# Kernel tuning notes

Hardware: AMD Instinct MI355X
Metric: run time of the kernel (lower is better)

Reference implementation:

```python
import jax, jax.numpy as jnp
import numpy as np

D_MODEL = 256; N_HEADS = 8; N_LEVELS = 4; N_POINTS = 4; NUM_ITER = 2
SHAPES = [(92, 160), (46, 80), (23, 40), (12, 20)]  # 4-level FPN, Len_in = 19560
LEN_IN = sum(h * w for h, w in SHAPES)
N_BATCH = 2


def _offset_bias():
    # faithful to _reset_parameters grid init of sampling_offsets.bias
    thetas = jnp.arange(N_HEADS, dtype=jnp.float32) * (2.0 * np.pi / N_HEADS)
    grid = jnp.stack([jnp.cos(thetas), jnp.sin(thetas)], -1)
    grid = grid / jnp.max(jnp.abs(grid), axis=-1, keepdims=True)
    grid = jnp.tile(grid[:, None, None, :], (1, N_LEVELS, N_POINTS, 1))
    grid = grid * (jnp.arange(N_POINTS, dtype=jnp.float32) + 1.0)[None, None, :, None]
    return grid.reshape(-1)


def setup_inputs() -> dict:
    key = jax.random.key(0)
    ks = jax.random.split(key, 12)
    N, Lq, d = N_BATCH, LEN_IN, D_MODEL
    s = 0.02
    return {
        "query0": jax.random.normal(ks[0], (N, Lq, d), jnp.float32),
        "query1": jax.random.normal(ks[1], (N, Lq, d), jnp.float32),
        "reference_points": jax.random.uniform(ks[2], (N, Lq, N_LEVELS, 2), jnp.float32),
        "input_flatten0": jax.random.normal(ks[3], (N, LEN_IN, d), jnp.float32),
        "input_flatten1": jax.random.normal(ks[4], (N, LEN_IN, d), jnp.float32),
        "input_spatial_shapes": jnp.array(SHAPES, jnp.int32),
        "input_level_start_index": jnp.array(np.cumsum([0] + [h * w for h, w in SHAPES[:-1]]), jnp.int32),
        "W_so": s * jax.random.normal(ks[5], (d, N_HEADS * N_LEVELS * N_POINTS * 2), jnp.float32),
        "b_so": _offset_bias(),
        "W_aw": s * jax.random.normal(ks[6], (d, N_HEADS * N_LEVELS * N_POINTS), jnp.float32),
        "b_aw": jnp.zeros((N_HEADS * N_LEVELS * N_POINTS,), jnp.float32),
        "W_v": s * jax.random.normal(ks[7], (d, d), jnp.float32),
        "b_v": jnp.zeros((d,), jnp.float32),
        "W_o": s * jax.random.normal(ks[8], (d, d), jnp.float32),
        "b_o": jnp.zeros((d,), jnp.float32),
        "W_agg": s * jax.random.normal(ks[9], (d * NUM_ITER, d), jnp.float32),
        "b_agg": jnp.zeros((d,), jnp.float32),
    }


def _sample_level(v_l, loc_l, H, W):
    # v_l: (N, nH, H*W, D); loc_l: (N, Lq, nH, P, 2) in [0,1]
    # bilinear, align_corners=False, zero padding (matches grid_sample fallback / CUDA kernel)
    x = loc_l[..., 0] * W - 0.5
    y = loc_l[..., 1] * H - 0.5
    x0 = jnp.floor(x); y0 = jnp.floor(y)

    def gather(xi, yi):
        inb = ((xi >= 0) & (xi <= W - 1) & (yi >= 0) & (yi <= H - 1)).astype(v_l.dtype)
        idx = (jnp.clip(yi, 0, H - 1) * W + jnp.clip(xi, 0, W - 1)).astype(jnp.int32)
        idx_t = jnp.transpose(idx, (0, 2, 1, 3))  # (N, nH, Lq, P)
        g = jax.vmap(jax.vmap(lambda vt, it: vt[it]))(v_l, idx_t)  # (N, nH, Lq, P, D)
        return g * jnp.transpose(inb, (0, 2, 1, 3))[..., None]

    def wt(w):
        return jnp.transpose(w, (0, 2, 1, 3))[..., None]

    return (wt((y0 + 1 - y) * (x0 + 1 - x)) * gather(x0, y0)
            + wt((y0 + 1 - y) * (x - x0)) * gather(x0 + 1, y0)
            + wt((y - y0) * (x0 + 1 - x)) * gather(x0, y0 + 1)
            + wt((y - y0) * (x - x0)) * gather(x0 + 1, y0 + 1))  # (N, nH, Lq, P, D)


def _ms_deform_attn(value, loc, attn, shapes, starts):
    # value: (N, Len_in, nH, D); loc: (N, Lq, nH, L, P, 2); attn: (N, Lq, nH, L, P)
    v = jnp.transpose(value, (0, 2, 1, 3))  # (N, nH, Len_in, D)
    acc = None
    for lvl in range(N_LEVELS):
        H, W = int(shapes[lvl, 0]), int(shapes[lvl, 1])
        s = int(starts[lvl])
        out_l = _sample_level(v[:, :, s:s + H * W], loc[:, :, :, lvl], H, W)
        a = jnp.transpose(attn[:, :, :, lvl], (0, 2, 1, 3))  # (N, nH, Lq, P)
        term = jnp.einsum('nhqpd,nhqp->nhqd', out_l, a)
        acc = term if acc is None else acc + term
    N, nH, Lq, D = acc.shape
    return jnp.transpose(acc, (0, 2, 1, 3)).reshape(N, Lq, nH * D)


def reference(query0, query1, reference_points, input_flatten0, input_flatten1,
              input_spatial_shapes, input_level_start_index,
              W_so, b_so, W_aw, b_aw, W_v, b_v, W_o, b_o, W_agg, b_agg):
    shapes = np.asarray(input_spatial_shapes)
    starts = np.asarray(input_level_start_index)
    N, Lq, d = query0.shape
    nH, L, P = N_HEADS, N_LEVELS, N_POINTS
    queries = [query0, query1]
    flats = [input_flatten0, input_flatten1]
    values, offs, aws = [], [], []
    for q, f in zip(queries, flats):
        values.append((f @ W_v + b_v).reshape(N, -1, nH, d // nH))
        offs.append((q @ W_so + b_so).reshape(N, Lq, nH, L, P, 2))
        aws.append((q @ W_aw + b_aw).reshape(N, Lq, nH, L * P))
    # joint softmax over num_iter * n_levels * n_points (the one-shot trick)
    aw_all = jax.nn.softmax(jnp.concatenate(aws, axis=-1), axis=-1)
    # (L, 2) normalizer = (W, H)
    normalizer = jnp.stack([input_spatial_shapes[..., 1], input_spatial_shapes[..., 0]], -1).astype(query0.dtype)
    outs = []
    for i in range(NUM_ITER):
        aw_i = aw_all[..., i * L * P:(i + 1) * L * P].reshape(N, Lq, nH, L, P)
        loc = reference_points[:, :, None, :, None, :] + offs[i] / normalizer[None, None, None, :, None, :]
        o = _ms_deform_attn(values[i], loc, aw_i, shapes, starts)
        outs.append(o @ W_o + b_o)
    return jnp.concatenate(outs, axis=-1) @ W_agg + b_agg
```

## Files before the change

kernel.cpp:

```cpp
#include <hip/hip_runtime.h>
#include <math.h>

#define NBATCH 2
#define LQ     19560
#define LEN    19560
#define NQ     (NBATCH * LQ)
#define DMODEL 256
#define NHEADS 8
#define HDIM   32
#define NLEV   4
#define NPTS   4
#define LDQS   384

typedef __bf16 bf16x8 __attribute__((ext_vector_type(8)));
typedef float  f32x4  __attribute__((ext_vector_type(4)));
typedef float  f32x2  __attribute__((ext_vector_type(2)));

__device__ inline float bf2f(unsigned short u) {
    return __uint_as_float(((unsigned int)u) << 16);
}
__device__ inline unsigned short f2bf(float f) {
    unsigned int u = __float_as_uint(f);
    u += 0x7FFFu + ((u >> 16) & 1u);
    return (unsigned short)(u >> 16);
}
__device__ inline f32x2 bfpair(unsigned int u) {
    f32x2 r;
    r.x = __uint_as_float(u << 16);
    r.y = __uint_as_float(u & 0xFFFF0000u);
    return r;
}

__global__ __launch_bounds__(256) void prep_all(
    const float* __restrict__ q0, const float* __restrict__ q1,
    const float* __restrict__ f0, const float* __restrict__ f1,
    const float* __restrict__ Wv, const float* __restrict__ Wso,
    const float* __restrict__ Waw, const float* __restrict__ bso,
    const float* __restrict__ baw,
    const float* __restrict__ Wo, const float* __restrict__ Wagg,
    const float* __restrict__ bo, const float* __restrict__ bagg,
    unsigned short* __restrict__ Qb0, unsigned short* __restrict__ Qb1,
    unsigned short* __restrict__ Fb0, unsigned short* __restrict__ Fb1,
    unsigned short* __restrict__ Wvt, unsigned short* __restrict__ Wsoawt,
    float* __restrict__ bsoaw,
    unsigned short* __restrict__ Wfcat, float* __restrict__ bfused)
{
    const int b = blockIdx.x;
    if (b < 19560) {
        const int tsel = b / 4890;
        const int x = b - tsel * 4890;
        const float* s = (tsel & 2) ? ((tsel & 1) ? f1 : f0) : ((tsel & 1) ? q1 : q0);
        unsigned short* d = (tsel & 2) ? ((tsel & 1) ? Fb1 : Fb0) : ((tsel & 1) ? Qb1 : Qb0);
        size_t i = ((size_t)x * 256 + threadIdx.x) * 8;
        float4 a = *(const float4*)(s + i);
        float4 c = *(const float4*)(s + i + 4);
        union { uint4 u; unsigned short h[8]; } t;
        t.h[0] = f2bf(a.x); t.h[1] = f2bf(a.y); t.h[2] = f2bf(a.z); t.h[3] = f2bf(a.w);
        t.h[4] = f2bf(c.x); t.h[5] = f2bf(c.y); t.h[6] = f2bf(c.z); t.h[7] = f2bf(c.w);
        *(uint4*)(d + i) = t.u;
    } else if (b < 19560 + 640) {
        int o = (b - 19560) * 256 + threadIdx.x;
        if (o < 65536) {
            int n = o >> 8, k = o & 255;
            Wvt[o] = f2bf(Wv[(size_t)k * 256 + n]);
        } else {
            int p = o - 65536;
            int n = p >> 8, k = p & 255;
            float v = (n < 256) ? Wso[(size_t)k * 256 + n] : Waw[(size_t)k * 128 + (n - 256)];
            Wsoawt[p] = f2bf(v);
        }
        if (o < 384) bsoaw[o] = (o < 256) ? bso[o] : baw[o - 256];
    } else {
        int k = b - 20200;
        int n = threadIdx.x;
        float s0 = 0.f, s1 = 0.f;
        for (int j = 0; j < 256; j++) {
            float w = Wo[k * 256 + j];
            s0 += w * Wagg[j * 256 + n];
            s1 += w * Wagg[(256 + j) * 256 + n];
        }
        Wfcat[(size_t)n * 512 + k]       = f2bf(s0);
        Wfcat[(size_t)n * 512 + 256 + k] = f2bf(s1);
        if (k == 0) {
            float bb = bagg[n];
            for (int j = 0; j < 256; j++)
                bb += bo[j] * (Wagg[j * 256 + n] + Wagg[(256 + j) * 256 + n]);
            bfused[n] = bb;
        }
    }
}

__global__ __launch_bounds__(256) void gemm_multi(
    const unsigned short* __restrict__ A0, const unsigned short* __restrict__ A1,
    const unsigned short* __restrict__ Bt, const float* __restrict__ bias,
    void* __restrict__ C0, void* __restrict__ C1,
    int M, int K, int lda, int N, int ldc, int mode)
{
    __shared__ __align__(16) unsigned short As[128 * 64];
    __shared__ __align__(16) unsigned short Bs[128 * 64];

    const int z = blockIdx.z;
    const unsigned short* A = z ? A1 : A0;
    void* Cv = z ? C1 : C0;

    const int tid  = threadIdx.x;
    const int w    = tid >> 6, lane = tid & 63;
    const int wm = w >> 1, wn = w & 1;
    const int m0 = blockIdx.y * 128, n0 = blockIdx.x * 128;
    const int lr = lane & 15, quad = lane >> 4;

    const int sr  = lane >> 3;
    const int scl = (lane & 7) ^ sr;
    const int colb = scl * 8;
    size_t arow[4], brow[4];
    #pragma unroll
    for (int j = 0; j < 4; j++) {
        int r = (w * 4 + j) * 8 + sr;
        int ra = m0 + r; if (ra > M - 1) ra = M - 1;
        arow[j] = (size_t)ra * lda;
        brow[j] = (size_t)(n0 + r) * K;
    }

    const f32x4 zero = {0.f, 0.f, 0.f, 0.f};
    f32x4 acc[4][4];
    #pragma unroll
    for (int i = 0; i < 4; i++)
        #pragma unroll
        for (int j = 0; j < 4; j++) acc[i][j] = zero;

    for (int t = 0; t < K; t += 64) {
        #pragma unroll
        for (int j = 0; j < 4; j++) {
            int lofs = __builtin_amdgcn_readfirstlane((w * 4 + j) * 1024);
            __builtin_amdgcn_global_load_lds(
                (const __attribute__((address_space(1))) void*)(A + arow[j] + t + colb),
                (__attribute__((address_space(3))) void*)((char*)As + lofs), 16, 0, 0);
            __builtin_amdgcn_global_load_lds(
                (const __attribute__((address_space(1))) void*)(Bt + brow[j] + t + colb),
                (__attribute__((address_space(3))) void*)((char*)Bs + lofs), 16, 0, 0);
        }
        __syncthreads();

        #pragma unroll
        for (int kk = 0; kk < 2; kk++) {
            bf16x8 af[4], bff[4];
            #pragma unroll
            for (int mi = 0; mi < 4; mi++) {
                int R = wm * 64 + mi * 16 + lr;
                int pc = ((kk * 4 + quad) ^ (lr & 7)) * 16;
                af[mi] = *(const bf16x8*)((const char*)As + R * 128 + pc);
            }
            #pragma unroll
            for (int ni = 0; ni < 4; ni++) {
                int R = wn * 64 + ni * 16 + lr;
                int pc = ((kk * 4 + quad) ^ (lr & 7)) * 16;
                bff[ni] = *(const bf16x8*)((const char*)Bs + R * 128 + pc);
            }
            #pragma unroll
            for (int mi = 0; mi < 4; mi++)
                #pragma unroll
                for (int ni = 0; ni < 4; ni++)
                    acc[mi][ni] = __builtin_amdgcn_mfma_f32_16x16x32_bf16(
                        af[mi], bff[ni], acc[mi][ni], 0, 0, 0);
        }
        __syncthreads();
    }

    float* Cf = (float*)Cv;
    unsigned short* Cb = (unsigned short*)Cv;
    #pragma unroll
    for (int mi = 0; mi < 4; mi++) {
        #pragma unroll
        for (int reg = 0; reg < 4; reg++) {
            int row = m0 + wm * 64 + mi * 16 + quad * 4 + reg;
            if (row >= M) continue;
            #pragma unroll
            for (int ni = 0; ni < 4; ni++) {
                int col = n0 + wn * 64 + ni * 16 + lr;
                float v = acc[mi][ni][reg];
                if (bias) v += bias[col];
                if (mode == 0) {
                    Cf[(size_t)row * ldc + col] = v;
                } else {
                    int n = row >= LQ ? 1 : 0;
                    int pos = row - n * LQ;
                    int h = col >> 5, d = col & 31;
                    Cb[((size_t)(n * NHEADS + h) * LEN + pos) * HDIM + d] = f2bf(v);
                }
            }
        }
    }
}

__global__ __launch_bounds__(256) void gemm_logits(
    const unsigned short* __restrict__ A0, const unsigned short* __restrict__ A1,
    const unsigned short* __restrict__ Bt,
    const float* __restrict__ bias,
    float* __restrict__ C0, float* __restrict__ C1, int M)
{
    __shared__ __align__(16) unsigned short As[128 * 64];
    __shared__ __align__(16) unsigned short Bs[128 * 64];

    const int tid  = threadIdx.x;
    const int w    = tid >> 6, lane = tid & 63;
    const int wm = w >> 1, wn = w & 1;
    const int m0 = blockIdx.x * 128;
    const int lr = lane & 15, quad = lane >> 4;

    const int sr  = lane >> 3;
    const int scl = (lane & 7) ^ sr;
    const int colb = scl * 8;
    size_t arow[4], brow[4];
    #pragma unroll
    for (int j = 0; j < 4; j++) {
        int r = (w * 4 + j) * 8 + sr;
        int ra = m0 + r; if (ra > M - 1) ra = M - 1;
        arow[j] = (size_t)ra * 256;
        brow[j] = (size_t)(256 + r) * 256;
    }

    const f32x4 zero = {0.f, 0.f, 0.f, 0.f};
    f32x4 acc[2][4][4];
    #pragma unroll
    for (int zz = 0; zz < 2; zz++)
        #pragma unroll
        for (int i = 0; i < 4; i++)
            #pragma unroll
            for (int j = 0; j < 4; j++) acc[zz][i][j] = zero;

    #pragma unroll
    for (int z = 0; z < 2; z++) {
        const unsigned short* A = z ? A1 : A0;
        for (int t = 0; t < 256; t += 64) {
            #pragma unroll
            for (int j = 0; j < 4; j++) {
                int lofs = __builtin_amdgcn_readfirstlane((w * 4 + j) * 1024);
                __builtin_amdgcn_global_load_lds(
                    (const __attribute__((address_space(1))) void*)(A + arow[j] + t + colb),
                    (__attribute__((address_space(3))) void*)((char*)As + lofs), 16, 0, 0);
                __builtin_amdgcn_global_load_lds(
                    (const __attribute__((address_space(1))) void*)(Bt + brow[j] + t + colb),
                    (__attribute__((address_space(3))) void*)((char*)Bs + lofs), 16, 0, 0);
            }
            __syncthreads();
            #pragma unroll
            for (int kk = 0; kk < 2; kk++) {
                bf16x8 af[4], bff[4];
                #pragma unroll
                for (int mi = 0; mi < 4; mi++) {
                    int R = wm * 64 + mi * 16 + lr;
                    int pc = ((kk * 4 + quad) ^ (lr & 7)) * 16;
                    af[mi] = *(const bf16x8*)((const char*)As + R * 128 + pc);
                }
                #pragma unroll
                for (int ni = 0; ni < 4; ni++) {
                    int R = wn * 64 + ni * 16 + lr;
                    int pc = ((kk * 4 + quad) ^ (lr & 7)) * 16;
                    bff[ni] = *(const bf16x8*)((const char*)Bs + R * 128 + pc);
                }
                #pragma unroll
                for (int mi = 0; mi < 4; mi++)
                    #pragma unroll
                    for (int ni = 0; ni < 4; ni++)
                        acc[z][mi][ni] = __builtin_amdgcn_mfma_f32_16x16x32_bf16(
                            af[mi], bff[ni], acc[z][mi][ni], 0, 0, 0);
            }
            __syncthreads();
        }
    }

    float bv[4];
    #pragma unroll
    for (int ni = 0; ni < 4; ni++) bv[ni] = bias[256 + wn * 64 + ni * 16 + lr];

    #pragma unroll
    for (int mi = 0; mi < 4; mi++) {
        #pragma unroll
        for (int reg = 0; reg < 4; reg++) {
            int row = m0 + wm * 64 + mi * 16 + quad * 4 + reg;
            #pragma unroll
            for (int ni = 0; ni < 4; ni++) {
                float a = acc[0][mi][ni][reg] + bv[ni];
                float c = acc[1][mi][ni][reg] + bv[ni];
                float m = fmaxf(a, c);
                #pragma unroll
                for (int d = 1; d < 16; d <<= 1) m = fmaxf(m, __shfl_xor(m, d));
                float ea = expf(a - m), ec = expf(c - m);
                float s = ea + ec;
                #pragma unroll
                for (int d = 1; d < 16; d <<= 1) s += __shfl_xor(s, d);
                float inv = 1.0f / s;
                if (row < M) {
                    int col = 256 + wn * 64 + ni * 16 + lr;
                    C0[(size_t)row * LDQS + col] = ea * inv;
                    C1[(size_t)row * LDQS + col] = ec * inv;
                }
            }
        }
    }
}

#define QCHUNK 64
#define CHUNKS ((LQ + QCHUNK - 1) / QCHUNK)

__global__ __launch_bounds__(256) void ms_sample(
    const unsigned short* __restrict__ V0, const unsigned short* __restrict__ V1,
    const float* __restrict__ QS0, const float* __restrict__ QS1,
    const float* __restrict__ refp, unsigned short* __restrict__ Ocat)
{
    __shared__ unsigned short Sidx[8][65][4];
    __shared__ float          Swt [8][65][4];

    const int b = blockIdx.x;
    const int h = b & 7;
    const int rest = b >> 3;
    const int chunk = rest % CHUNKS;
    const int inn   = rest / CHUNKS;
    const int n  = inn & 1;
    const int it = inn >> 1;

    const int tid = threadIdx.x;
    const int ql  = tid >> 2;
    const int lj  = tid & 3;
    const int qraw = chunk * QCHUNK + ql;
    const bool valid = qraw < LQ;
    const int q  = valid ? qraw : LQ - 1;
    const int nq = n * LQ + q;

    const unsigned short* __restrict__ val = it ? V1 : V0;
    const float* __restrict__ QS = it ? QS1 : QS0;
    const unsigned short* __restrict__ vb2 =
        val + (size_t)(n * NHEADS + h) * LEN * HDIM;

    const int Hs[4] = {92, 46, 23, 12};
    const int Ws[4] = {160, 80, 40, 20};
    const int Ss[4] = {0, 14720, 18400, 19320};

    const float* prow = QS + (size_t)nq * LDQS;
    const int dl = lj << 3;
    const unsigned short* __restrict__ vdl = vb2 + dl;

    f32x2 acc[4];
    #pragma unroll
    for (int i = 0; i < 4; i++) acc[i] = (f32x2){0.f, 0.f};

    auto corner = [&](unsigned int eo, float wgt) {
        const uint4 c = *(const uint4*)(vdl + eo);
        const f32x2 w2 = {wgt, wgt};
        acc[0] += w2 * bfpair(c.x);
        acc[1] += w2 * bfpair(c.y);
        acc[2] += w2 * bfpair(c.z);
        acc[3] += w2 * bfpair(c.w);
    };

    #pragma unroll
    for (int pass = 0; pass < 2; pass++) {
        {
            const int lvl = lj >> 1;
            const int l   = (pass << 1) | lvl;
            const int kb  = (lj & 1) << 1;
            const int H = Hs[l], W = Ws[l], S = Ss[l];
            const float2 rp = *(const float2*)(refp + (size_t)nq * 8 + l * 2);
            const float fx = rp.x * (float)W - 0.5f;
            const float fy = rp.y * (float)H - 0.5f;
            const float4 off = *(const float4*)(prow + (h << 5) + l * 8 + (kb << 1));
            const float2 aw2 = *(const float2*)(prow + 256 + (h << 4) + (l << 2) + kb);
            const float oxs[2] = {off.x, off.z};
            const float oys[2] = {off.y, off.w};
            const float avs[2] = {aw2.x, aw2.y};
            #pragma unroll
            for (int i = 0; i < 2; i++) {
                const float x = fx + oxs[i];
                const float y = fy + oys[i];
                const float x0f = floorf(x), y0f = floorf(y);
                const int x0 = (int)x0f, y0 = (int)y0f;
                const float wx1 = x - x0f, wy1 = y - y0f;
                const float wx0 = 1.0f - wx1, wy0 = 1.0f - wy1;
                const int xc0 = min(max(x0, 0), W - 1);
                const int xc1 = min(max(x0 + 1, 0), W - 1);
                const int yc0 = min(max(y0, 0), H - 1);
                const int yc1 = min(max(y0 + 1, 0), H - 1);
                const float a = avs[i];
                const float ay0 = ((unsigned int)y0 < (unsigned int)H) ? a * wy0 : 0.f;
                const float ay1 = ((unsigned int)(y0 + 1) < (unsigned int)H) ? a * wy1 : 0.f;
                const float mx0 = ((unsigned int)x0 < (unsigned int)W) ? wx0 : 0.f;
                const float mx1 = ((unsigned int)(x0 + 1) < (unsigned int)W) ? wx1 : 0.f;
                const int r0 = S + yc0 * W, r1 = S + yc1 * W;
                union { uint2 u; unsigned short s4[4]; } ip;
                ip.s4[0] = (unsigned short)(r0 + xc0);
                ip.s4[1] = (unsigned short)(r0 + xc1);
                ip.s4[2] = (unsigned short)(r1 + xc0);
                ip.s4[3] = (unsigned short)(r1 + xc1);
                const int sp = (lvl << 2) + kb + i;
                *(uint2*)&Sidx[sp][ql][0] = ip.u;
                float4 w4 = make_float4(ay0 * mx0, ay0 * mx1, ay1 * mx0, ay1 * mx1);
                *(float4*)&Swt[sp][ql][0] = w4;
            }
        }
        __syncthreads();

        #pragma unroll
        for (int p = 0; p < 8; p++) {
            const uint2 i2 = *(const uint2*)&Sidx[p][ql][0];
            const float4 w4 = *(const float4*)&Swt[p][ql][0];
            corner((i2.x & 0xFFFFu) << 5, w4.x);
            corner((i2.x >> 16) << 5, w4.y);
            corner((i2.y & 0xFFFFu) << 5, w4.z);
            corner((i2.y >> 16) << 5, w4.w);
        }
        if (pass == 0) __syncthreads();
    }

    if (valid) {
        union { uint4 u; unsigned short s[8]; } t;
        #pragma unroll
        for (int i = 0; i < 4; i++) {
            t.s[2 * i]     = f2bf(acc[i].x);
            t.s[2 * i + 1] = f2bf(acc[i].y);
        }
        *(uint4*)&Ocat[(size_t)nq * 512 + it * 256 + h * HDIM + dl] = t.u;
    }
}

extern "C" void kernel_launch(void* const* d_in, const int* in_sizes, int n_in,
                              void* d_out, int out_size, void* d_ws, size_t ws_size,
                              hipStream_t stream)
{
    const float* q0    = (const float*)d_in[0];
    const float* q1    = (const float*)d_in[1];
    const float* refp  = (const float*)d_in[2];
    const float* f0    = (const float*)d_in[3];
    const float* f1    = (const float*)d_in[4];
    const float* W_so  = (const float*)d_in[7];
    const float* b_so  = (const float*)d_in[8];
    const float* W_aw  = (const float*)d_in[9];
    const float* b_aw  = (const float*)d_in[10];
    const float* W_v   = (const float*)d_in[11];
    const float* b_v   = (const float*)d_in[12];
    const float* W_o   = (const float*)d_in[13];
    const float* b_o   = (const float*)d_in[14];
    const float* W_agg = (const float*)d_in[15];
    const float* b_agg = (const float*)d_in[16];
    float* out = (float*)d_out;

    float* ws = (float*)d_ws;
    float* QS0 = ws;
    float* QS1 = QS0 + (size_t)NQ * LDQS;
    unsigned short* V0   = (unsigned short*)(QS1 + (size_t)NQ * LDQS);
    unsigned short* V1   = V0 + (size_t)NQ * 256;
    unsigned short* Ocat = V1 + (size_t)NQ * 256;
    unsigned short* Wvt    = Ocat + (size_t)NQ * 512;
    unsigned short* Wsoawt = Wvt + 65536;
    unsigned short* Wfcat  = Wsoawt + 98304;
    float* bsoaw = (float*)(Wfcat + 131072);
    float* bfus  = bsoaw + 384;

    unsigned short* Qb0 = V0;
    unsigned short* Qb1 = V1;
    unsigned short* Fb0 = Ocat;
    unsigned short* Fb1 = Ocat + (size_t)NQ * 256;

    const int MB = (NQ + 127) / 128;
    dim3 blk(256);

    prep_all<<<20456, blk, 0, stream>>>(
        q0, q1, f0, f1, W_v, W_so, W_aw, b_so, b_aw, W_o, W_agg, b_o, b_agg,
        Qb0, Qb1, Fb0, Fb1, Wvt, Wsoawt, bsoaw, Wfcat, bfus);

    gemm_multi<<<dim3(2, MB, 2), blk, 0, stream>>>(
        Qb0, Qb1, Wsoawt, bsoaw, QS0, QS1, NQ, 256, 256, 384, LDQS, 0);

    gemm_logits<<<MB, blk, 0, stream>>>(
        Qb0, Qb1, Wsoawt, bsoaw, QS0, QS1, NQ);

    gemm_multi<<<dim3(2, MB, 2), blk, 0, stream>>>(
        Fb0, Fb1, Wvt, b_v, V0, V1, NQ, 256, 256, 256, 256, 2);

    ms_sample<<<2 * 2 * CHUNKS * 8, blk, 0, stream>>>(V0, V1, QS0, QS1, refp, Ocat);

    gemm_multi<<<dim3(2, MB, 1), blk, 0, stream>>>(
        Ocat, Ocat, Wfcat, bfus, out, out, NQ, 512, 512, 256, 256, 0);
}
```

Measured before the change: 564.9 us.

## Merge offset and value GEMMs into one launch and stage bf16 queries inside QS

The sampling-offset GEMM and the value-projection GEMM now run as a single four-slice launch. The bf16 copy of each query is written into the unused logit columns of its own QS row, so the later logits kernel reads it from there and the V buffers no longer double as query scratch. The sampler now computes all 16 level/point sample slots in one setup phase with a single barrier instead of two passes. The output GEMM becomes a specialized kernel with constant sizes. The intent is fewer launches, fewer barriers and fewer runtime branches. The cost is larger LDS arrays in the sampler and a tighter dependence on buffer aliasing and kernel ordering.

```diff
diff --git a/kernel.cpp b/kernel.cpp
--- a/kernel.cpp
+++ b/kernel.cpp
@@ -16,9 +16,6 @@
 typedef float  f32x4  __attribute__((ext_vector_type(4)));
 typedef float  f32x2  __attribute__((ext_vector_type(2)));
 
-__device__ inline float bf2f(unsigned short u) {
-    return __uint_as_float(((unsigned int)u) << 16);
-}
 __device__ inline unsigned short f2bf(float f) {
     unsigned int u = __float_as_uint(f);
     u += 0x7FFFu + ((u >> 16) & 1u);
@@ -57,7 +54,12 @@
         union { uint4 u; unsigned short h[8]; } t;
         t.h[0] = f2bf(a.x); t.h[1] = f2bf(a.y); t.h[2] = f2bf(a.z); t.h[3] = f2bf(a.w);
         t.h[4] = f2bf(c.x); t.h[5] = f2bf(c.y); t.h[6] = f2bf(c.z); t.h[7] = f2bf(c.w);
-        *(uint4*)(d + i) = t.u;
+        if (tsel & 2) {
+            *(uint4*)(d + i) = t.u;
+        } else {
+            size_t row = i >> 8; int c8 = (int)(i & 255);
+            *(uint4*)(d + row * 768 + 512 + c8) = t.u;
+        }
     } else if (b < 19560 + 640) {
         int o = (b - 19560) * 256 + threadIdx.x;
         if (o < 65536) {
@@ -90,18 +92,24 @@
     }
 }
 
-__global__ __launch_bounds__(256) void gemm_multi(
-    const unsigned short* __restrict__ A0, const unsigned short* __restrict__ A1,
-    const unsigned short* __restrict__ Bt, const float* __restrict__ bias,
-    void* __restrict__ C0, void* __restrict__ C1,
-    int M, int K, int lda, int N, int ldc, int mode)
+__global__ __launch_bounds__(256) void gemm_mid(
+    const unsigned short* __restrict__ Qa0, const unsigned short* __restrict__ Qa1,
+    const unsigned short* __restrict__ Fb0, const unsigned short* __restrict__ Fb1,
+    const unsigned short* __restrict__ Wsoawt, const unsigned short* __restrict__ Wvt,
+    const float* __restrict__ bsoaw, const float* __restrict__ bv,
+    float* __restrict__ QS0, float* __restrict__ QS1,
+    unsigned short* __restrict__ V0, unsigned short* __restrict__ V1)
 {
     __shared__ __align__(16) unsigned short As[128 * 64];
     __shared__ __align__(16) unsigned short Bs[128 * 64];
 
     const int z = blockIdx.z;
-    const unsigned short* A = z ? A1 : A0;
-    void* Cv = z ? C1 : C0;
+    const int isOff = (z < 2);
+    const int zz = z & 1;
+    const unsigned short* A = isOff ? (zz ? Qa1 : Qa0) : (zz ? Fb1 : Fb0);
+    const unsigned short* Bt = isOff ? Wsoawt : Wvt;
+    const float* bias = isOff ? bsoaw : bv;
+    const int lda = isOff ? 768 : 256;
 
     const int tid  = threadIdx.x;
     const int w    = tid >> 6, lane = tid & 63;
@@ -116,9 +124,9 @@
     #pragma unroll
     for (int j = 0; j < 4; j++) {
         int r = (w * 4 + j) * 8 + sr;
-        int ra = m0 + r; if (ra > M - 1) ra = M - 1;
+        int ra = m0 + r; if (ra > NQ - 1) ra = NQ - 1;
         arow[j] = (size_t)ra * lda;
-        brow[j] = (size_t)(n0 + r) * K;
+        brow[j] = (size_t)(n0 + r) * 256;
     }
 
     const f32x4 zero = {0.f, 0.f, 0.f, 0.f};
@@ -128,7 +136,7 @@
         #pragma unroll
         for (int j = 0; j < 4; j++) acc[i][j] = zero;
 
-    for (int t = 0; t < K; t += 64) {
+    for (int t = 0; t < 256; t += 64) {
         #pragma unroll
         for (int j = 0; j < 4; j++) {
             int lofs = __builtin_amdgcn_readfirstlane((w * 4 + j) * 1024);
@@ -166,21 +174,20 @@
         __syncthreads();
     }
 
-    float* Cf = (float*)Cv;
-    unsigned short* Cb = (unsigned short*)Cv;
+    float* Cf = isOff ? (zz ? QS1 : QS0) : nullptr;
+    unsigned short* Cb = isOff ? nullptr : (zz ? V1 : V0);
     #pragma unroll
     for (int mi = 0; mi < 4; mi++) {
         #pragma unroll
         for (int reg = 0; reg < 4; reg++) {
             int row = m0 + wm * 64 + mi * 16 + quad * 4 + reg;
-            if (row >= M) continue;
+            if (row >= NQ) continue;
             #pragma unroll
             for (int ni = 0; ni < 4; ni++) {
                 int col = n0 + wn * 64 + ni * 16 + lr;
-                float v = acc[mi][ni][reg];
-                if (bias) v += bias[col];
-                if (mode == 0) {
-                    Cf[(size_t)row * ldc + col] = v;
+                float v = acc[mi][ni][reg] + bias[col];
+                if (isOff) {
+                    Cf[(size_t)row * LDQS + col] = v;
                 } else {
                     int n = row >= LQ ? 1 : 0;
                     int pos = row - n * LQ;
@@ -193,10 +200,10 @@
 }
 
 __global__ __launch_bounds__(256) void gemm_logits(
-    const unsigned short* __restrict__ A0, const unsigned short* __restrict__ A1,
+    const unsigned short* __restrict__ Qa0, const unsigned short* __restrict__ Qa1,
     const unsigned short* __restrict__ Bt,
     const float* __restrict__ bias,
-    float* __restrict__ C0, float* __restrict__ C1, int M)
+    float* __restrict__ C0, float* __restrict__ C1)
 {
     __shared__ __align__(16) unsigned short As[128 * 64];
     __shared__ __align__(16) unsigned short Bs[128 * 64];
@@ -214,8 +221,8 @@
     #pragma unroll
     for (int j = 0; j < 4; j++) {
         int r = (w * 4 + j) * 8 + sr;
-        int ra = m0 + r; if (ra > M - 1) ra = M - 1;
-        arow[j] = (size_t)ra * 256;
+        int ra = m0 + r; if (ra > NQ - 1) ra = NQ - 1;
+        arow[j] = (size_t)ra * 768;
         brow[j] = (size_t)(256 + r) * 256;
     }
 
@@ -230,7 +237,7 @@
 
     #pragma unroll
     for (int z = 0; z < 2; z++) {
-        const unsigned short* A = z ? A1 : A0;
+        const unsigned short* A = z ? Qa1 : Qa0;
         for (int t = 0; t < 256; t += 64) {
             #pragma unroll
             for (int j = 0; j < 4; j++) {
@@ -290,7 +297,7 @@
                 #pragma unroll
                 for (int d = 1; d < 16; d <<= 1) s += __shfl_xor(s, d);
                 float inv = 1.0f / s;
-                if (row < M) {
+                if (row < NQ) {
                     int col = 256 + wn * 64 + ni * 16 + lr;
                     C0[(size_t)row * LDQS + col] = ea * inv;
                     C1[(size_t)row * LDQS + col] = ec * inv;
@@ -308,8 +315,8 @@
     const float* __restrict__ QS0, const float* __restrict__ QS1,
     const float* __restrict__ refp, unsigned short* __restrict__ Ocat)
 {
-    __shared__ unsigned short Sidx[8][65][4];
-    __shared__ float          Swt [8][65][4];
+    __shared__ unsigned short Sidx[16][65][4];
+    __shared__ float          Swt [16][65][4];
 
     const int b = blockIdx.x;
     const int h = b & 7;
@@ -337,6 +344,48 @@
     const int Ss[4] = {0, 14720, 18400, 19320};
 
     const float* prow = QS + (size_t)nq * LDQS;
+
+    {
+        const int H = Hs[lj], W = Ws[lj], S = Ss[lj];
+        const float4 o0 = *(const float4*)(prow + (h << 5) + lj * 8);
+        const float4 o1 = *(const float4*)(prow + (h << 5) + lj * 8 + 4);
+        const float4 a4 = *(const float4*)(prow + 256 + (h << 4) + lj * 4);
+        const float2 rp = *(const float2*)(refp + (size_t)nq * 8 + lj * 2);
+        const float fx = rp.x * (float)W - 0.5f;
+        const float fy = rp.y * (float)H - 0.5f;
+        const float oxs[4] = {o0.x, o0.z, o1.x, o1.z};
+        const float oys[4] = {o0.y, o0.w, o1.y, o1.w};
+        const float avs[4] = {a4.x, a4.y, a4.z, a4.w};
+        #pragma unroll
+        for (int k = 0; k < NPTS; k++) {
+            const float x = fx + oxs[k];
+            const float y = fy + oys[k];
+            const float x0f = floorf(x), y0f = floorf(y);
+            const int x0 = (int)x0f, y0 = (int)y0f;
+            const float wx1 = x - x0f, wy1 = y - y0f;
+            const float wx0 = 1.0f - wx1, wy0 = 1.0f - wy1;
+            const int xc0 = min(max(x0, 0), W - 1);
+            const int xc1 = min(max(x0 + 1, 0), W - 1);
+            const int yc0 = min(max(y0, 0), H - 1);
+            const int yc1 = min(max(y0 + 1, 0), H - 1);
+            const float a = avs[k];
+            const float ay0 = ((unsigned int)y0 < (unsigned int)H) ? a * wy0 : 0.f;
+            const float ay1 = ((unsigned int)(y0 + 1) < (unsigned int)H) ? a * wy1 : 0.f;
+            const float mx0 = ((unsigned int)x0 < (unsigned int)W) ? wx0 : 0.f;
+            const float mx1 = ((unsigned int)(x0 + 1) < (unsigned int)W) ? wx1 : 0.f;
+            const int r0 = S + yc0 * W, r1 = S + yc1 * W;
+            union { uint2 u; unsigned short s4[4]; } ip;
+            ip.s4[0] = (unsigned short)(r0 + xc0);
+            ip.s4[1] = (unsigned short)(r0 + xc1);
+            ip.s4[2] = (unsigned short)(r1 + xc0);
+            ip.s4[3] = (unsigned short)(r1 + xc1);
+            *(uint2*)&Sidx[lj * 4 + k][ql][0] = ip.u;
+            float4 w4 = make_float4(ay0 * mx0, ay0 * mx1, ay1 * mx0, ay1 * mx1);
+            *(float4*)&Swt[lj * 4 + k][ql][0] = w4;
+        }
+    }
+    __syncthreads();
+
     const int dl = lj << 3;
     const unsigned short* __restrict__ vdl = vb2 + dl;
 
@@ -354,61 +403,13 @@
     };
 
     #pragma unroll
-    for (int pass = 0; pass < 2; pass++) {
-        {
-            const int lvl = lj >> 1;
-            const int l   = (pass << 1) | lvl;
-            const int kb  = (lj & 1) << 1;
-            const int H = Hs[l], W = Ws[l], S = Ss[l];
-            const float2 rp = *(const float2*)(refp + (size_t)nq * 8 + l * 2);
-            const float fx = rp.x * (float)W - 0.5f;
-            const float fy = rp.y * (float)H - 0.5f;
-            const float4 off = *(const float4*)(prow + (h << 5) + l * 8 + (kb << 1));
-            const float2 aw2 = *(const float2*)(prow + 256 + (h << 4) + (l << 2) + kb);
-            const float oxs[2] = {off.x, off.z};
-            const float oys[2] = {off.y, off.w};
-            const float avs[2] = {aw2.x, aw2.y};
-            #pragma unroll
-            for (int i = 0; i < 2; i++) {
-                const float x = fx + oxs[i];
-                const float y = fy + oys[i];
-                const float x0f = floorf(x), y0f = floorf(y);
-                const int x0 = (int)x0f, y0 = (int)y0f;
-                const float wx1 = x - x0f, wy1 = y - y0f;
-                const float wx0 = 1.0f - wx1, wy0 = 1.0f - wy1;
-                const int xc0 = min(max(x0, 0), W - 1);
-                const int xc1 = min(max(x0 + 1, 0), W - 1);
-                const int yc0 = min(max(y0, 0), H - 1);
-                const int yc1 = min(max(y0 + 1, 0), H - 1);
-                const float a = avs[i];
-                const float ay0 = ((unsigned int)y0 < (unsigned int)H) ? a * wy0 : 0.f;
-                const float ay1 = ((unsigned int)(y0 + 1) < (unsigned int)H) ? a * wy1 : 0.f;
-                const float mx0 = ((unsigned int)x0 < (unsigned int)W) ? wx0 : 0.f;
-                const float mx1 = ((unsigned int)(x0 + 1) < (unsigned int)W) ? wx1 : 0.f;
-                const int r0 = S + yc0 * W, r1 = S + yc1 * W;
-                union { uint2 u; unsigned short s4[4]; } ip;
-                ip.s4[0] = (unsigned short)(r0 + xc0);
-                ip.s4[1] = (unsigned short)(r0 + xc1);
-                ip.s4[2] = (unsigned short)(r1 + xc0);
-                ip.s4[3] = (unsigned short)(r1 + xc1);
-                const int sp = (lvl << 2) + kb + i;
-                *(uint2*)&Sidx[sp][ql][0] = ip.u;
-                float4 w4 = make_float4(ay0 * mx0, ay0 * mx1, ay1 * mx0, ay1 * mx1);
-                *(float4*)&Swt[sp][ql][0] = w4;
-            }
-        }
-        __syncthreads();
-
-        #pragma unroll
-        for (int p = 0; p < 8; p++) {
-            const uint2 i2 = *(const uint2*)&Sidx[p][ql][0];
-            const float4 w4 = *(const float4*)&Swt[p][ql][0];
-            corner((i2.x & 0xFFFFu) << 5, w4.x);
-            corner((i2.x >> 16) << 5, w4.y);
-            corner((i2.y & 0xFFFFu) << 5, w4.z);
-            corner((i2.y >> 16) << 5, w4.w);
-        }
-        if (pass == 0) __syncthreads();
+    for (int p = 0; p < 16; p++) {
+        const uint2 i2 = *(const uint2*)&Sidx[p][ql][0];
+        const float4 w4 = *(const float4*)&Swt[p][ql][0];
+        corner((i2.x & 0xFFFFu) << 5, w4.x);
+        corner((i2.x >> 16) << 5, w4.y);
+        corner((i2.y & 0xFFFFu) << 5, w4.z);
+        corner((i2.y >> 16) << 5, w4.w);
     }
 
     if (valid) {
@@ -419,6 +420,91 @@
             t.s[2 * i + 1] = f2bf(acc[i].y);
         }
         *(uint4*)&Ocat[(size_t)nq * 512 + it * 256 + h * HDIM + dl] = t.u;
+    }
+}
+
+__global__ __launch_bounds__(256) void gemm_tail(
+    const unsigned short* __restrict__ A, const unsigned short* __restrict__ Bt,
+    const float* __restrict__ bias, float* __restrict__ C)
+{
+    __shared__ __align__(16) unsigned short As[128 * 64];
+    __shared__ __align__(16) unsigned short Bs[128 * 64];
+
+    const int tid  = threadIdx.x;
+    const int w    = tid >> 6, lane = tid & 63;
+    const int wm = w >> 1, wn = w & 1;
+    const int m0 = blockIdx.y * 128, n0 = blockIdx.x * 128;
+    const int lr = lane & 15, quad = lane >> 4;
+
+    const int sr  = lane >> 3;
+    const int scl = (lane & 7) ^ sr;
+    const int colb = scl * 8;
+    size_t arow[4], brow[4];
+    #pragma unroll
+    for (int j = 0; j < 4; j++) {
+        int r = (w * 4 + j) * 8 + sr;
+        int ra = m0 + r; if (ra > NQ - 1) ra = NQ - 1;
+        arow[j] = (size_t)ra * 512;
+        brow[j] = (size_t)(n0 + r) * 512;
+    }
+
+    const f32x4 zero = {0.f, 0.f, 0.f, 0.f};
+    f32x4 acc[4][4];
+    #pragma unroll
+    for (int i = 0; i < 4; i++)
+        #pragma unroll
+        for (int j = 0; j < 4; j++) acc[i][j] = zero;
+
+    for (int t = 0; t < 512; t += 64) {
+        #pragma unroll
+        for (int j = 0; j < 4; j++) {
+            int lofs = __builtin_amdgcn_readfirstlane((w * 4 + j) * 1024);
+            __builtin_amdgcn_global_load_lds(
+                (const __attribute__((address_space(1))) void*)(A + arow[j] + t + colb),
+                (__attribute__((address_space(3))) void*)((char*)As + lofs), 16, 0, 0);
+            __builtin_amdgcn_global_load_lds(
+                (const __attribute__((address_space(1))) void*)(Bt + brow[j] + t + colb),
+                (__attribute__((address_space(3))) void*)((char*)Bs + lofs), 16, 0, 0);
+        }
+        __syncthreads();
+
+        #pragma unroll
+        for (int kk = 0; kk < 2; kk++) {
+            bf16x8 af[4], bff[4];
+            #pragma unroll
+            for (int mi = 0; mi < 4; mi++) {
+                int R = wm * 64 + mi * 16 + lr;
+                int pc = ((kk * 4 + quad) ^ (lr & 7)) * 16;
+                af[mi] = *(const bf16x8*)((const char*)As + R * 128 + pc);
+            }
+            #pragma unroll
+            for (int ni = 0; ni < 4; ni++) {
+                int R = wn * 64 + ni * 16 + lr;
+                int pc = ((kk * 4 + quad) ^ (lr & 7)) * 16;
+                bff[ni] = *(const bf16x8*)((const char*)Bs + R * 128 + pc);
+            }
+            #pragma unroll
+            for (int mi = 0; mi < 4; mi++)
+                #pragma unroll
+                for (int ni = 0; ni < 4; ni++)
+                    acc[mi][ni] = __builtin_amdgcn_mfma_f32_16x16x32_bf16(
+                        af[mi], bff[ni], acc[mi][ni], 0, 0, 0);
+        }
+        __syncthreads();
+    }
+
+    #pragma unroll
+    for (int mi = 0; mi < 4; mi++) {
+        #pragma unroll
+        for (int reg = 0; reg < 4; reg++) {
+            int row = m0 + wm * 64 + mi * 16 + quad * 4 + reg;
+            if (row >= NQ) continue;
+            #pragma unroll
+            for (int ni = 0; ni < 4; ni++) {
+                int col = n0 + wn * 64 + ni * 16 + lr;
+                C[(size_t)row * 256 + col] = acc[mi][ni][reg] + bias[col];
+            }
+        }
     }
 }
 
@@ -455,10 +541,12 @@
     float* bsoaw = (float*)(Wfcat + 131072);
     float* bfus  = bsoaw + 384;
 
-    unsigned short* Qb0 = V0;
-    unsigned short* Qb1 = V1;
+    unsigned short* Qb0 = (unsigned short*)QS0;
+    unsigned short* Qb1 = (unsigned short*)QS1;
     unsigned short* Fb0 = Ocat;
     unsigned short* Fb1 = Ocat + (size_t)NQ * 256;
+    const unsigned short* Qa0 = (const unsigned short*)QS0 + 512;
+    const unsigned short* Qa1 = (const unsigned short*)QS1 + 512;
 
     const int MB = (NQ + 127) / 128;
     dim3 blk(256);
@@ -467,17 +555,12 @@
         q0, q1, f0, f1, W_v, W_so, W_aw, b_so, b_aw, W_o, W_agg, b_o, b_agg,
         Qb0, Qb1, Fb0, Fb1, Wvt, Wsoawt, bsoaw, Wfcat, bfus);
 
-    gemm_multi<<<dim3(2, MB, 2), blk, 0, stream>>>(
-        Qb0, Qb1, Wsoawt, bsoaw, QS0, QS1, NQ, 256, 256, 384, LDQS, 0);
-
-    gemm_logits<<<MB, blk, 0, stream>>>(
-        Qb0, Qb1, Wsoawt, bsoaw, QS0, QS1, NQ);
-
-    gemm_multi<<<dim3(2, MB, 2), blk, 0, stream>>>(
-        Fb0, Fb1, Wvt, b_v, V0, V1, NQ, 256, 256, 256, 256, 2);
+    gemm_mid<<<dim3(2, MB, 4), blk, 0, stream>>>(
+        Qa0, Qa1, Fb0, Fb1, Wsoawt, Wvt, bsoaw, b_v, QS0, QS1, V0, V1);
+
+    gemm_logits<<<MB, blk, 0, stream>>>(Qa0, Qa1, Wsoawt, bsoaw, QS0, QS1);
 
     ms_sample<<<2 * 2 * CHUNKS * 8, blk, 0, stream>>>(V0, V1, QS0, QS1, refp, Ocat);
 
-    gemm_multi<<<dim3(2, MB, 1), blk, 0, stream>>>(
-        Ocat, Ocat, Wfcat, bfus, out, out, NQ, 512, 512, 256, 256, 0);
-}
+    gemm_tail<<<dim3(2, MB, 1), blk, 0, stream>>>(Ocat, Wfcat, bfus, out);
+}
```

After: 480.0 us. 1.18x faster.
